# Kernel tuning notes

Measured on AMD Instinct MI355X. Metric: run time of the kernel, lower is better.

The kernel has to match this reference:

```python
import jax, jax.numpy as jnp
import numpy as np

V = 2562
DEG = 8
NNZ = V * DEG
B, FIN, FOUT, K = 1, 8, 16, 5
X = Y = Z = 8


def setup_inputs() -> dict:
    key = jax.random.key(0)
    k1, k2, k3, k4, k5 = jax.random.split(key, 5)
    inputs = jax.random.normal(k1, (B, FIN, V, X, Y, Z), dtype=jnp.float32)
    # COO sparse Laplacian: each vertex has DEG entries (valid row indices)
    lap_rows = jnp.repeat(jnp.arange(V, dtype=jnp.int32), DEG)
    lap_cols = jax.random.randint(k2, (NNZ,), 0, V, dtype=jnp.int32)
    lap_vals = jax.random.normal(k3, (NNZ,), dtype=jnp.float32) * 0.1
    std = np.sqrt(2.0 / (FIN * K)).astype(np.float32)
    weight = jax.random.normal(k4, (K, FIN, FOUT), dtype=jnp.float32) * std
    bias = jnp.full((FOUT,), 0.01, dtype=jnp.float32)
    return {"inputs": inputs, "lap_rows": lap_rows, "lap_cols": lap_cols,
            "lap_vals": lap_vals, "weight": weight, "bias": bias}


def _spmv(vals, rows, cols, x):
    # sparse [V,V] @ dense [V,D] via gather + segment_sum
    return jax.ops.segment_sum(vals[:, None] * x[cols], rows, num_segments=V)


def reference(inputs, lap_rows, lap_cols, lap_vals, weight, bias):
    # x0: [V, Fin*B*X*Y*Z]
    x0 = jnp.transpose(inputs, (2, 1, 0, 3, 4, 5)).reshape(V, FIN * B * X * Y * Z)
    xs = [x0]
    if K > 1:
        x1 = _spmv(lap_vals, lap_rows, lap_cols, x0)
        xs.append(x1)
        for _ in range(2, K):
            x2 = 2.0 * _spmv(lap_vals, lap_rows, lap_cols, x1) - x0
            xs.append(x2)
            x0, x1 = x1, x2
    cheb = jnp.stack(xs, 0).reshape(K, V, FIN, B, X, Y, Z)
    # matmul over (K, Fin): out [B, Fout, V, X, Y, Z]
    out = jnp.einsum('kvfbxyz,kfo->bovxyz', cheb, weight)
    out = out + bias[None, :, None, None, None, None]
    return out
```

## Files before the change

kernel.cpp:

```cpp
#include <hip/hip_runtime.h>
#include <hip/hip_bf16.h>

constexpr int V_    = 2562;
constexpr int DEG_  = 8;
constexpr int FIN_  = 8;
constexpr int FOUT_ = 16;
constexpr int S_    = 512;
constexpr int VS_   = V_ * S_;
constexpr int VP_   = 2564;
constexpr int LSTR  = 12;
constexpr long INT_PLANE = (long)S_ * VP_;
constexpr int TPB   = 1024;
constexpr int NV    = 3;

__device__ __forceinline__ float4 ld4(const float* p) {
    return *reinterpret_cast<const float4*>(p);
}
__device__ __forceinline__ void st4(float* p, float4 v) {
    *reinterpret_cast<float4*>(p) = v;
}

__global__ __launch_bounds__(256)
void transpose_k(const float* __restrict__ src, float* __restrict__ dst,
                 int M, int N, long srcZ, long dstZ, int dstStride)
{
    __shared__ float tile[64][65];
    const long zs = (long)blockIdx.z * srcZ;
    const long zd = (long)blockIdx.z * dstZ;
    const int n0 = blockIdx.x * 64;
    const int m0 = blockIdx.y * 64;
    const int t  = threadIdx.x;
    const int q  = t & 15;
    const int r  = t >> 4;

#pragma unroll
    for (int i = 0; i < 4; ++i) {
        const int m = m0 + r + i * 16;
        const int n = n0 + q * 4;
        if (m < M && n < N) {
            const float4 x = ld4(src + zs + (long)m * N + n);
            tile[r + i * 16][q * 4 + 0] = x.x;
            tile[r + i * 16][q * 4 + 1] = x.y;
            tile[r + i * 16][q * 4 + 2] = x.z;
            tile[r + i * 16][q * 4 + 3] = x.w;
        }
    }
    __syncthreads();
#pragma unroll
    for (int i = 0; i < 4; ++i) {
        const int n = n0 + r + i * 16;
        const int m = m0 + q * 4;
        if (n < N && (m + 4) <= dstStride) {
            const float4 x = make_float4(tile[q * 4 + 0][r + i * 16],
                                         tile[q * 4 + 1][r + i * 16],
                                         tile[q * 4 + 2][r + i * 16],
                                         tile[q * 4 + 3][r + i * 16]);
            st4(dst + zd + (long)n * dstStride + m, x);
        }
    }
}

__global__ __launch_bounds__(TPB)
void cheb_rec(const float* __restrict__ inT,
              const int*   __restrict__ cols,
              const float* __restrict__ vals,
              __hip_bfloat16* __restrict__ cheb)
{
    extern __shared__ float cur[];
    const int s = blockIdx.x;
    const int t = threadIdx.x;

    {
        const int f = t & 7;
        const int cb = t >> 3;
        const float* plane = inT + (long)f * INT_PLANE + (long)s * VP_;
        for (int c = cb; c < VP_ / 4; c += TPB / 8) {
            const float4 x = ld4(plane + c * 4);
            cur[(c * 4 + 0) * LSTR + f] = x.x;
            cur[(c * 4 + 1) * LSTR + f] = x.y;
            cur[(c * 4 + 2) * LSTR + f] = x.z;
            cur[(c * 4 + 3) * LSTR + f] = x.w;
        }
    }
    __syncthreads();

    float xp[NV][8];
#pragma unroll
    for (int j = 0; j < NV; ++j) {
        const int v = (t + j * TPB < V_) ? (t + j * TPB) : 0;
        const float4 lo = ld4(&cur[v * LSTR]);
        const float4 hi = ld4(&cur[v * LSTR + 4]);
        xp[j][0] = lo.x; xp[j][1] = lo.y; xp[j][2] = lo.z; xp[j][3] = lo.w;
        xp[j][4] = hi.x; xp[j][5] = hi.y; xp[j][6] = hi.z; xp[j][7] = hi.w;
    }

#pragma unroll 1
    for (int k = 1; k < 5; ++k) {
        float xk[NV][8];
#pragma unroll
        for (int j = 0; j < NV; ++j) {
            const bool valid = (t + j * TPB) < V_;
            const int v = valid ? (t + j * TPB) : 0;
            int off = v * 8;
            asm volatile("" : "+v"(off));
            const int4   ca = *reinterpret_cast<const int4*>(cols + off);
            const int4   cb = *reinterpret_cast<const int4*>(cols + off + 4);
            const float4 wa = ld4(vals + off);
            const float4 wb = ld4(vals + off + 4);
            const int   cc[8] = {ca.x, ca.y, ca.z, ca.w, cb.x, cb.y, cb.z, cb.w};
            const float ww[8] = {wa.x, wa.y, wa.z, wa.w, wb.x, wb.y, wb.z, wb.w};

            float a[8];
#pragma unroll
            for (int e = 0; e < 8; ++e) a[e] = 0.f;
#pragma unroll
            for (int n = 0; n < 8; ++n) {
                const float* p = &cur[cc[n] * LSTR];
                const float4 lo = ld4(p);
                const float4 hi = ld4(p + 4);
                const float w = ww[n];
                a[0] = fmaf(w, lo.x, a[0]); a[1] = fmaf(w, lo.y, a[1]);
                a[2] = fmaf(w, lo.z, a[2]); a[3] = fmaf(w, lo.w, a[3]);
                a[4] = fmaf(w, hi.x, a[4]); a[5] = fmaf(w, hi.y, a[5]);
                a[6] = fmaf(w, hi.z, a[6]); a[7] = fmaf(w, hi.w, a[7]);
            }
#pragma unroll
            for (int e = 0; e < 8; ++e)
                xk[j][e] = (k == 1) ? a[e] : fmaf(2.f, a[e], -xp[j][e]);

            if (valid) {
                const long pb = ((long)(k - 1) * S_ + s) * FIN_;
#pragma unroll
                for (int f = 0; f < 8; ++f)
                    cheb[(pb + f) * VP_ + v] = __float2bfloat16(xk[j][f]);
            }

            if (k < 4) {
                const float4 lo = ld4(&cur[v * LSTR]);
                const float4 hi = ld4(&cur[v * LSTR + 4]);
                xp[j][0] = lo.x; xp[j][1] = lo.y; xp[j][2] = lo.z; xp[j][3] = lo.w;
                xp[j][4] = hi.x; xp[j][5] = hi.y; xp[j][6] = hi.z; xp[j][7] = hi.w;
            }
        }
        if (k < 4) {
            __syncthreads();
#pragma unroll
            for (int j = 0; j < NV; ++j) {
                const int vr = t + j * TPB;
                if (vr < V_) {
                    st4(&cur[vr * LSTR],
                        make_float4(xk[j][0], xk[j][1], xk[j][2], xk[j][3]));
                    st4(&cur[vr * LSTR + 4],
                        make_float4(xk[j][4], xk[j][5], xk[j][6], xk[j][7]));
                }
            }
            __syncthreads();
        }
    }
}

__global__ __launch_bounds__(TPB)
void proj(const float* __restrict__ in,
          const __hip_bfloat16* __restrict__ cheb,
          const float* __restrict__ W,
          const float* __restrict__ bias,
          float* __restrict__ out)
{
    __shared__ float x0t[FIN_][64][17];
    __shared__ float ot[64][17];
    const int v0 = blockIdx.x * 64;
    const int s0 = blockIdx.y * 16;
    const int t  = threadIdx.x;

    {
        const int sv = t & 15;
        const int vv = t >> 4;
        const int vg = (v0 + vv < V_) ? (v0 + vv) : (V_ - 1);
#pragma unroll
        for (int f = 0; f < FIN_; ++f)
            x0t[f][vv][sv] = in[(long)f * VS_ + (long)vg * S_ + s0 + sv];
    }
    __syncthreads();

    const int tv = t & 63;
    const int ts = t >> 6;
    const int vg = (v0 + tv < V_) ? (v0 + tv) : (V_ - 1);

    float acc[16];
#pragma unroll
    for (int o = 0; o < 16; ++o) acc[o] = bias[o];

#pragma unroll
    for (int f = 0; f < FIN_; ++f) {
        const float xv = x0t[f][tv][ts];
#pragma unroll
        for (int o = 0; o < 16; ++o)
            acc[o] = fmaf(W[f * 16 + o], xv, acc[o]);
    }
#pragma unroll
    for (int k = 1; k < 5; ++k) {
#pragma unroll
        for (int f = 0; f < FIN_; ++f) {
            const long pb = ((long)(k - 1) * S_ + (s0 + ts)) * FIN_ + f;
            const float xv = __bfloat162float(cheb[pb * VP_ + vg]);
#pragma unroll
            for (int o = 0; o < 16; ++o)
                acc[o] = fmaf(W[(k * 8 + f) * 16 + o], xv, acc[o]);
        }
    }

    const int sv = t & 15;
    const int vv = t >> 4;
    const bool wval = (v0 + vv) < V_;
#pragma unroll 1
    for (int o = 0; o < 16; ++o) {
        __syncthreads();
        ot[tv][ts] = acc[o];
        __syncthreads();
        if (wval)
            out[(long)o * VS_ + (long)(v0 + vv) * S_ + s0 + sv] = ot[vv][sv];
    }
}

extern "C" void kernel_launch(void* const* d_in, const int* in_sizes, int n_in,
                              void* d_out, int out_size, void* d_ws, size_t ws_size,
                              hipStream_t stream) {
    const float* in   = (const float*)d_in[0];
    const int*   cols = (const int*)d_in[2];
    const float* vals = (const float*)d_in[3];
    const float* W    = (const float*)d_in[4];
    const float* bias = (const float*)d_in[5];
    float* out = (float*)d_out;

    float* inT = out;
    __hip_bfloat16* cheb = (__hip_bfloat16*)d_ws;

    (void)hipFuncSetAttribute((const void*)cheb_rec,
                              hipFuncAttributeMaxDynamicSharedMemorySize,
                              VP_ * LSTR * (int)sizeof(float));

    transpose_k<<<dim3(8, 41, 8), 256, 0, stream>>>(
        in, inT, V_, S_, (long)VS_, INT_PLANE, VP_);

    cheb_rec<<<dim3(S_), TPB, VP_ * LSTR * (int)sizeof(float), stream>>>(
        inT, cols, vals, cheb);

    proj<<<dim3(41, 32), TPB, 0, stream>>>(in, cheb, W, bias, out);
}
```

Before: 231.9 us.

## Fuse Chebyshev recurrence with projection using fp16 LDS state and packed half2 FMAs

Folds the per-k weight projection into the recurrence kernel, so the Chebyshev terms are never written to global memory. Each block now emits a 16-channel output tile in fp16, which a final transpose kernel converts back to fp32 in the output layout. The LDS state changes from fp32 with a 12-float stride to packed half2 (16 bytes per vertex), and the SpMV uses __hfma2. This removes the large bf16 cheb write and read-back, halves LDS footprint and traffic, and doubles FMA throughput per instruction. In exchange, fp16 accumulation of the recurrence and an fp16 output intermediate lose precision, and each thread holds 48 extra accumulator registers, which raises register pressure.

```diff
diff --git a/kernel.cpp b/kernel.cpp
--- a/kernel.cpp
+++ b/kernel.cpp
@@ -1,14 +1,12 @@
 #include <hip/hip_runtime.h>
-#include <hip/hip_bf16.h>
+#include <hip/hip_fp16.h>
 
 constexpr int V_    = 2562;
-constexpr int DEG_  = 8;
 constexpr int FIN_  = 8;
 constexpr int FOUT_ = 16;
 constexpr int S_    = 512;
 constexpr int VS_   = V_ * S_;
 constexpr int VP_   = 2564;
-constexpr int LSTR  = 12;
 constexpr long INT_PLANE = (long)S_ * VP_;
 constexpr int TPB   = 1024;
 constexpr int NV    = 3;
@@ -19,10 +17,24 @@
 __device__ __forceinline__ void st4(float* p, float4 v) {
     *reinterpret_cast<float4*>(p) = v;
 }
+__device__ __forceinline__ unsigned h2bits(__half2 h) {
+    union { __half2 h; unsigned u; } c; c.h = h; return c.u;
+}
+__device__ __forceinline__ __half2 bits2h(unsigned u) {
+    union { unsigned u; __half2 h; } c; c.u = u; return c.h;
+}
+__device__ __forceinline__ unsigned packh2(float e, float o) {
+    return h2bits(__halves2half2(__float2half(e), __float2half(o)));
+}
+__device__ __forceinline__ ushort f2h_bits(float x) {
+    __half h = __float2half(x);
+    return *reinterpret_cast<ushort*>(&h);
+}
 
 __global__ __launch_bounds__(256)
-void transpose_k(const float* __restrict__ src, float* __restrict__ dst,
-                 int M, int N, long srcZ, long dstZ, int dstStride)
+void transpose_g(const float* __restrict__ src, float* __restrict__ dst,
+                 int M, int N, int srcStride, int dstStride,
+                 long srcZ, long dstZ)
 {
     __shared__ float tile[64][65];
     const long zs = (long)blockIdx.z * srcZ;
@@ -38,7 +50,7 @@
         const int m = m0 + r + i * 16;
         const int n = n0 + q * 4;
         if (m < M && n < N) {
-            const float4 x = ld4(src + zs + (long)m * N + n);
+            const float4 x = ld4(src + zs + (long)m * srcStride + n);
             tile[r + i * 16][q * 4 + 0] = x.x;
             tile[r + i * 16][q * 4 + 1] = x.y;
             tile[r + i * 16][q * 4 + 2] = x.z;
@@ -60,43 +72,107 @@
     }
 }
 
+__global__ __launch_bounds__(256)
+void transpose_h(const ushort* __restrict__ src, float* __restrict__ dst,
+                 int M, int N, int srcStride, int dstStride,
+                 long srcZ, long dstZ)
+{
+    __shared__ float tile[64][65];
+    const long zs = (long)blockIdx.z * srcZ;
+    const long zd = (long)blockIdx.z * dstZ;
+    const int n0 = blockIdx.x * 64;
+    const int m0 = blockIdx.y * 64;
+    const int t  = threadIdx.x;
+    const int q  = t & 15;
+    const int r  = t >> 4;
+
+#pragma unroll
+    for (int i = 0; i < 4; ++i) {
+        const int m = m0 + r + i * 16;
+        const int n = n0 + q * 4;
+        if (m < M && n < N) {
+            const uint2 u = *reinterpret_cast<const uint2*>(
+                src + zs + (long)m * srcStride + n);
+            const __half2 h0 = bits2h(u.x);
+            const __half2 h1 = bits2h(u.y);
+            tile[r + i * 16][q * 4 + 0] = __half2float(__low2half(h0));
+            tile[r + i * 16][q * 4 + 1] = __half2float(__high2half(h0));
+            tile[r + i * 16][q * 4 + 2] = __half2float(__low2half(h1));
+            tile[r + i * 16][q * 4 + 3] = __half2float(__high2half(h1));
+        }
+    }
+    __syncthreads();
+#pragma unroll
+    for (int i = 0; i < 4; ++i) {
+        const int n = n0 + r + i * 16;
+        const int m = m0 + q * 4;
+        if (n < N && (m + 4) <= dstStride) {
+            const float4 x = make_float4(tile[q * 4 + 0][r + i * 16],
+                                         tile[q * 4 + 1][r + i * 16],
+                                         tile[q * 4 + 2][r + i * 16],
+                                         tile[q * 4 + 3][r + i * 16]);
+            st4(dst + zd + (long)n * dstStride + m, x);
+        }
+    }
+}
+
 __global__ __launch_bounds__(TPB)
-void cheb_rec(const float* __restrict__ inT,
-              const int*   __restrict__ cols,
-              const float* __restrict__ vals,
-              __hip_bfloat16* __restrict__ cheb)
+void cheb_proj(const float* __restrict__ inT,
+               const int*   __restrict__ cols,
+               const float* __restrict__ vals,
+               const float* __restrict__ W,
+               const float* __restrict__ bias,
+               ushort* __restrict__ y)
 {
-    extern __shared__ float cur[];
+    __shared__ uint4 cur4[VP_];
+    unsigned* curd = reinterpret_cast<unsigned*>(cur4);
     const int s = blockIdx.x;
     const int t = threadIdx.x;
 
     {
-        const int f = t & 7;
-        const int cb = t >> 3;
-        const float* plane = inT + (long)f * INT_PLANE + (long)s * VP_;
-        for (int c = cb; c < VP_ / 4; c += TPB / 8) {
-            const float4 x = ld4(plane + c * 4);
-            cur[(c * 4 + 0) * LSTR + f] = x.x;
-            cur[(c * 4 + 1) * LSTR + f] = x.y;
-            cur[(c * 4 + 2) * LSTR + f] = x.z;
-            cur[(c * 4 + 3) * LSTR + f] = x.w;
+        const int d  = t & 3;
+        const float* p0 = inT + (long)(2 * d)     * INT_PLANE + (long)s * VP_;
+        const float* p1 = inT + (long)(2 * d + 1) * INT_PLANE + (long)s * VP_;
+        for (int c = t >> 2; c < VP_ / 4; c += TPB / 4) {
+            const float4 xe = ld4(p0 + c * 4);
+            const float4 xo = ld4(p1 + c * 4);
+            curd[(c * 4 + 0) * 4 + d] = packh2(xe.x, xo.x);
+            curd[(c * 4 + 1) * 4 + d] = packh2(xe.y, xo.y);
+            curd[(c * 4 + 2) * 4 + d] = packh2(xe.z, xo.z);
+            curd[(c * 4 + 3) * 4 + d] = packh2(xe.w, xo.w);
         }
     }
     __syncthreads();
 
-    float xp[NV][8];
+    __half2 xp[NV][4];
+    float acc[NV][16];
 #pragma unroll
     for (int j = 0; j < NV; ++j) {
         const int v = (t + j * TPB < V_) ? (t + j * TPB) : 0;
-        const float4 lo = ld4(&cur[v * LSTR]);
-        const float4 hi = ld4(&cur[v * LSTR + 4]);
-        xp[j][0] = lo.x; xp[j][1] = lo.y; xp[j][2] = lo.z; xp[j][3] = lo.w;
-        xp[j][4] = hi.x; xp[j][5] = hi.y; xp[j][6] = hi.z; xp[j][7] = hi.w;
-    }
+        const uint4 r = cur4[v];
+        xp[j][0] = bits2h(r.x); xp[j][1] = bits2h(r.y);
+        xp[j][2] = bits2h(r.z); xp[j][3] = bits2h(r.w);
+        float xf[8];
+#pragma unroll
+        for (int e = 0; e < 4; ++e) {
+            xf[2 * e]     = __half2float(__low2half(xp[j][e]));
+            xf[2 * e + 1] = __half2float(__high2half(xp[j][e]));
+        }
+#pragma unroll
+        for (int o = 0; o < 16; ++o) {
+            float a = bias[o];
+#pragma unroll
+            for (int f = 0; f < 8; ++f)
+                a = fmaf(W[f * 16 + o], xf[f], a);
+            acc[j][o] = a;
+        }
+    }
+
+    const __half2 two2 = __half2half2(__float2half(2.0f));
 
 #pragma unroll 1
     for (int k = 1; k < 5; ++k) {
-        float xk[NV][8];
+        __half2 xk[NV][4];
 #pragma unroll
         for (int j = 0; j < NV; ++j) {
             const bool valid = (t + j * TPB) < V_;
@@ -110,36 +186,40 @@
             const int   cc[8] = {ca.x, ca.y, ca.z, ca.w, cb.x, cb.y, cb.z, cb.w};
             const float ww[8] = {wa.x, wa.y, wa.z, wa.w, wb.x, wb.y, wb.z, wb.w};
 
-            float a[8];
-#pragma unroll
-            for (int e = 0; e < 8; ++e) a[e] = 0.f;
+            __half2 a4[4];
+#pragma unroll
+            for (int e = 0; e < 4; ++e) a4[e] = bits2h(0u);
 #pragma unroll
             for (int n = 0; n < 8; ++n) {
-                const float* p = &cur[cc[n] * LSTR];
-                const float4 lo = ld4(p);
-                const float4 hi = ld4(p + 4);
-                const float w = ww[n];
-                a[0] = fmaf(w, lo.x, a[0]); a[1] = fmaf(w, lo.y, a[1]);
-                a[2] = fmaf(w, lo.z, a[2]); a[3] = fmaf(w, lo.w, a[3]);
-                a[4] = fmaf(w, hi.x, a[4]); a[5] = fmaf(w, hi.y, a[5]);
-                a[6] = fmaf(w, hi.z, a[6]); a[7] = fmaf(w, hi.w, a[7]);
-            }
-#pragma unroll
-            for (int e = 0; e < 8; ++e)
-                xk[j][e] = (k == 1) ? a[e] : fmaf(2.f, a[e], -xp[j][e]);
-
-            if (valid) {
-                const long pb = ((long)(k - 1) * S_ + s) * FIN_;
-#pragma unroll
-                for (int f = 0; f < 8; ++f)
-                    cheb[(pb + f) * VP_ + v] = __float2bfloat16(xk[j][f]);
+                const uint4 rr = cur4[cc[n]];
+                const __half2 w2 = __half2half2(__float2half(ww[n]));
+                a4[0] = __hfma2(w2, bits2h(rr.x), a4[0]);
+                a4[1] = __hfma2(w2, bits2h(rr.y), a4[1]);
+                a4[2] = __hfma2(w2, bits2h(rr.z), a4[2]);
+                a4[3] = __hfma2(w2, bits2h(rr.w), a4[3]);
+            }
+#pragma unroll
+            for (int e = 0; e < 4; ++e)
+                xk[j][e] = (k == 1) ? a4[e]
+                                    : __hfma2(two2, a4[e], __hneg2(xp[j][e]));
+
+            float xf[8];
+#pragma unroll
+            for (int e = 0; e < 4; ++e) {
+                xf[2 * e]     = __half2float(__low2half(xk[j][e]));
+                xf[2 * e + 1] = __half2float(__high2half(xk[j][e]));
+            }
+#pragma unroll
+            for (int f = 0; f < 8; ++f) {
+#pragma unroll
+                for (int o = 0; o < 16; ++o)
+                    acc[j][o] = fmaf(W[(k * 8 + f) * 16 + o], xf[f], acc[j][o]);
             }
 
             if (k < 4) {
-                const float4 lo = ld4(&cur[v * LSTR]);
-                const float4 hi = ld4(&cur[v * LSTR + 4]);
-                xp[j][0] = lo.x; xp[j][1] = lo.y; xp[j][2] = lo.z; xp[j][3] = lo.w;
-                xp[j][4] = hi.x; xp[j][5] = hi.y; xp[j][6] = hi.z; xp[j][7] = hi.w;
+                const uint4 rr = cur4[v];
+                xp[j][0] = bits2h(rr.x); xp[j][1] = bits2h(rr.y);
+                xp[j][2] = bits2h(rr.z); xp[j][3] = bits2h(rr.w);
             }
         }
         if (k < 4) {
@@ -147,78 +227,22 @@
 #pragma unroll
             for (int j = 0; j < NV; ++j) {
                 const int vr = t + j * TPB;
-                if (vr < V_) {
-                    st4(&cur[vr * LSTR],
-                        make_float4(xk[j][0], xk[j][1], xk[j][2], xk[j][3]));
-                    st4(&cur[vr * LSTR + 4],
-                        make_float4(xk[j][4], xk[j][5], xk[j][6], xk[j][7]));
-                }
+                if (vr < V_)
+                    cur4[vr] = make_uint4(h2bits(xk[j][0]), h2bits(xk[j][1]),
+                                          h2bits(xk[j][2]), h2bits(xk[j][3]));
             }
             __syncthreads();
         }
     }
-}
-
-__global__ __launch_bounds__(TPB)
-void proj(const float* __restrict__ in,
-          const __hip_bfloat16* __restrict__ cheb,
-          const float* __restrict__ W,
-          const float* __restrict__ bias,
-          float* __restrict__ out)
-{
-    __shared__ float x0t[FIN_][64][17];
-    __shared__ float ot[64][17];
-    const int v0 = blockIdx.x * 64;
-    const int s0 = blockIdx.y * 16;
-    const int t  = threadIdx.x;
-
-    {
-        const int sv = t & 15;
-        const int vv = t >> 4;
-        const int vg = (v0 + vv < V_) ? (v0 + vv) : (V_ - 1);
-#pragma unroll
-        for (int f = 0; f < FIN_; ++f)
-            x0t[f][vv][sv] = in[(long)f * VS_ + (long)vg * S_ + s0 + sv];
-    }
-    __syncthreads();
-
-    const int tv = t & 63;
-    const int ts = t >> 6;
-    const int vg = (v0 + tv < V_) ? (v0 + tv) : (V_ - 1);
-
-    float acc[16];
-#pragma unroll
-    for (int o = 0; o < 16; ++o) acc[o] = bias[o];
-
-#pragma unroll
-    for (int f = 0; f < FIN_; ++f) {
-        const float xv = x0t[f][tv][ts];
-#pragma unroll
-        for (int o = 0; o < 16; ++o)
-            acc[o] = fmaf(W[f * 16 + o], xv, acc[o]);
-    }
-#pragma unroll
-    for (int k = 1; k < 5; ++k) {
-#pragma unroll
-        for (int f = 0; f < FIN_; ++f) {
-            const long pb = ((long)(k - 1) * S_ + (s0 + ts)) * FIN_ + f;
-            const float xv = __bfloat162float(cheb[pb * VP_ + vg]);
+
+#pragma unroll
+    for (int j = 0; j < NV; ++j) {
+        const int v = t + j * TPB;
+        if (v < V_) {
 #pragma unroll
             for (int o = 0; o < 16; ++o)
-                acc[o] = fmaf(W[(k * 8 + f) * 16 + o], xv, acc[o]);
-        }
-    }
-
-    const int sv = t & 15;
-    const int vv = t >> 4;
-    const bool wval = (v0 + vv) < V_;
-#pragma unroll 1
-    for (int o = 0; o < 16; ++o) {
-        __syncthreads();
-        ot[tv][ts] = acc[o];
-        __syncthreads();
-        if (wval)
-            out[(long)o * VS_ + (long)(v0 + vv) * S_ + s0 + sv] = ot[vv][sv];
+                y[((long)o * S_ + s) * VP_ + v] = f2h_bits(acc[j][o]);
+        }
     }
 }
 
@@ -232,18 +256,14 @@
     const float* bias = (const float*)d_in[5];
     float* out = (float*)d_out;
 
-    float* inT = out;
-    __hip_bfloat16* cheb = (__hip_bfloat16*)d_ws;
-
-    (void)hipFuncSetAttribute((const void*)cheb_rec,
-                              hipFuncAttributeMaxDynamicSharedMemorySize,
-                              VP_ * LSTR * (int)sizeof(float));
-
-    transpose_k<<<dim3(8, 41, 8), 256, 0, stream>>>(
-        in, inT, V_, S_, (long)VS_, INT_PLANE, VP_);
-
-    cheb_rec<<<dim3(S_), TPB, VP_ * LSTR * (int)sizeof(float), stream>>>(
-        inT, cols, vals, cheb);
-
-    proj<<<dim3(41, 32), TPB, 0, stream>>>(in, cheb, W, bias, out);
-}
+    float*  inT = out;
+    ushort* y   = (ushort*)d_ws;
+
+    transpose_g<<<dim3(8, 41, 8), 256, 0, stream>>>(
+        in, inT, V_, S_, S_, VP_, (long)VS_, INT_PLANE);
+
+    cheb_proj<<<dim3(S_), TPB, 0, stream>>>(inT, cols, vals, W, bias, y);
+
+    transpose_h<<<dim3(41, 8, 16), 256, 0, stream>>>(
+        y, out, S_, V_, VP_, S_, INT_PLANE, (long)VS_);
+}
```

New measurement: 369.0 us. 59.2% more time.
